# Performance work log

Measured on AMD Instinct MI355X. Metric: run time of the kernel, lower is better.

## Reference

```python
import jax, jax.numpy as jnp
import numpy as np

EPS_BN = 1e-3   # nn.BatchNorm1d(eps=0.001)
LAMDA = 1e-5    # Point_Attentation.lamda


def _bn(x, g, b, m, v):
    # inference-mode BatchNorm1d over last dim
    return (x - m) * (g * jax.lax.rsqrt(v + EPS_BN)) + b


def _forward(features_low, features_high,
             bott_W, bott_b, bott_gamma, bott_beta, bott_mean, bott_var,
             qkv_W, qkv_gamma, qkv_beta, qkv_mean, qkv_var,
             mlp_W, mlp_gamma, mlp_beta, mlp_mean, mlp_var,
             fus_W, fus_b, fus_gamma, fus_beta, fus_mean, fus_var,
             batch_size):
    N, C = features_low.shape
    B = batch_size
    n = N // B  # points per batch segment (equal-length segments)

    # ---- Point_Attentation: per-point channel mean, var over channels / (n-1) ----
    x = features_low
    mean = jnp.mean(x, axis=-1, keepdims=True)
    d = x - mean
    var = jnp.sum(d * d, axis=-1, keepdims=True) / (n - 1)
    e_t = d * d / (4.0 * (var + LAMDA)) + 0.5
    x = x + jax.nn.sigmoid(e_t) * x

    for i in range(3):
        y = jax.nn.relu(_bn(x @ bott_W[2 * i] + bott_b[2 * i],
                            bott_gamma[2 * i], bott_beta[2 * i], bott_mean[2 * i], bott_var[2 * i]))
        y = jax.nn.relu(_bn(y @ bott_W[2 * i + 1] + bott_b[2 * i + 1],
                            bott_gamma[2 * i + 1], bott_beta[2 * i + 1], bott_mean[2 * i + 1], bott_var[2 * i + 1]))
        x = x + y

    # ---- fusion: per-batch QKV attention between low (x) and high features ----
    low = x.reshape(B, n, C)
    high = features_high.reshape(B, n, C)

    q = _bn(jnp.einsum('bnc,cd->bnd', low, qkv_W[0]), qkv_gamma[0], qkv_beta[0], qkv_mean[0], qkv_var[0])
    k = _bn(jnp.einsum('bnc,cd->bnd', high, qkv_W[1]), qkv_gamma[1], qkv_beta[1], qkv_mean[1], qkv_var[1])
    v = _bn(jnp.einsum('bnc,cd->bnd', high, qkv_W[2]), qkv_gamma[2], qkv_beta[2], qkv_mean[2], qkv_var[2])

    scale = 1.0 / jnp.sqrt(jnp.asarray(256.0, dtype=q.dtype))  # normal_dim = 256
    attn = jax.nn.softmax(jnp.einsum('bqc,bkc->bqk', q, k) * scale, axis=-1)
    ao = jnp.einsum('bqk,bkc->bqc', attn, v)

    # mlp: (Linear no-bias -> BN -> Dropout(eval=id) -> ReLU) x2
    h = jax.nn.relu(_bn(jnp.einsum('bnc,cd->bnd', ao, mlp_W[0]), mlp_gamma[0], mlp_beta[0], mlp_mean[0], mlp_var[0]))
    h = jax.nn.relu(_bn(jnp.einsum('bnc,cd->bnd', h, mlp_W[1]), mlp_gamma[1], mlp_beta[1], mlp_mean[1], mlp_var[1]))

    # linear_fusion: Linear(2C->C, bias) -> BN -> ReLU
    cat = jnp.concatenate([low, h], axis=-1)  # [B, n, 2C]
    out = jax.nn.relu(_bn(jnp.einsum('bnc,cd->bnd', cat, fus_W) + fus_b, fus_gamma, fus_beta, fus_mean, fus_var))
    return out.reshape(N, C)


def setup_inputs() -> dict:
    key = jax.random.key(0)
    ks = jax.random.split(key, 16)
    N, C, B = 16384, 256, 4
    s = 0.05
    d = {}
    d['features_low'] = jax.random.normal(ks[0], (N, C), jnp.float32)
    d['features_high'] = jax.random.normal(ks[1], (N, C), jnp.float32)
    d['bott_W'] = jax.random.normal(ks[2], (6, C, C), jnp.float32) * s
    d['bott_b'] = jnp.zeros((6, C), jnp.float32)
    d['bott_gamma'] = jnp.ones((6, C), jnp.float32)
    d['bott_beta'] = jnp.zeros((6, C), jnp.float32)
    d['bott_mean'] = jnp.zeros((6, C), jnp.float32)
    d['bott_var'] = jnp.ones((6, C), jnp.float32)
    d['qkv_W'] = jax.random.normal(ks[3], (3, C, C), jnp.float32) * s
    d['qkv_gamma'] = jnp.ones((3, C), jnp.float32)
    d['qkv_beta'] = jnp.zeros((3, C), jnp.float32)
    d['qkv_mean'] = jnp.zeros((3, C), jnp.float32)
    d['qkv_var'] = jnp.ones((3, C), jnp.float32)
    d['mlp_W'] = jax.random.normal(ks[4], (2, C, C), jnp.float32) * s
    d['mlp_gamma'] = jnp.ones((2, C), jnp.float32)
    d['mlp_beta'] = jnp.zeros((2, C), jnp.float32)
    d['mlp_mean'] = jnp.zeros((2, C), jnp.float32)
    d['mlp_var'] = jnp.ones((2, C), jnp.float32)
    d['fus_W'] = jax.random.normal(ks[5], (2 * C, C), jnp.float32) * s
    d['fus_b'] = jnp.zeros((C,), jnp.float32)
    d['fus_gamma'] = jnp.ones((C,), jnp.float32)
    d['fus_beta'] = jnp.zeros((C,), jnp.float32)
    d['fus_mean'] = jnp.zeros((C,), jnp.float32)
    d['fus_var'] = jnp.ones((C,), jnp.float32)
    d['batch_size'] = B
    return d


def reference(features_low, features_high,
              bott_W, bott_b, bott_gamma, bott_beta, bott_mean, bott_var,
              qkv_W, qkv_gamma, qkv_beta, qkv_mean, qkv_var,
              mlp_W, mlp_gamma, mlp_beta, mlp_mean, mlp_var,
              fus_W, fus_b, fus_gamma, fus_beta, fus_mean, fus_var,
              batch_size):
    return _forward(features_low, features_high,
                    bott_W, bott_b, bott_gamma, bott_beta, bott_mean, bott_var,
                    qkv_W, qkv_gamma, qkv_beta, qkv_mean, qkv_var,
                    mlp_W, mlp_gamma, mlp_beta, mlp_mean, mlp_var,
                    fus_W, fus_b, fus_gamma, fus_beta, fus_mean, fus_var,
                    batch_size)
```

## Files before the change

### kernel.cpp

```cpp
#include <hip/hip_runtime.h>
#include <cstdint>
#include <cstddef>

typedef float v4f __attribute__((ext_vector_type(4)));
typedef float v2f __attribute__((ext_vector_type(2)));
typedef short v8s __attribute__((ext_vector_type(8)));
typedef unsigned short v4u __attribute__((ext_vector_type(4)));

typedef unsigned short ubf;

#define NPTS 16384
#define CD   256
#define NBAT 4
#define NPB  4096

__device__ __forceinline__ float bf2f(ubf u) {
    union { unsigned u; float f; } c; c.u = ((unsigned)u) << 16; return c.f;
}
__device__ __forceinline__ ubf f2bf(float f) {
    union { float f; unsigned u; } c; c.f = f;
    unsigned u = c.u;
    u += 0x7fffu + ((u >> 16) & 1u);
    return (ubf)(u >> 16);
}

__global__ void k_wtrans(const float* __restrict__ bott, const float* __restrict__ qkv,
                         const float* __restrict__ mlp, const float* __restrict__ fus,
                         ubf* __restrict__ wt) {
    const int z = blockIdx.z;
    const float* src; int K; size_t doff;
    if (z < 6)       { src = bott + (size_t)z * 65536;       K = 256; doff = (size_t)z * 65536; }
    else if (z < 9)  { src = qkv  + (size_t)(z - 6) * 65536; K = 256; doff = (size_t)z * 65536; }
    else if (z < 11) { src = mlp  + (size_t)(z - 9) * 65536; K = 256; doff = (size_t)z * 65536; }
    else             { src = fus;                            K = 512; doff = (size_t)11 * 65536; }
    const int kt = blockIdx.y * 32, nt = blockIdx.x * 32;
    if (kt >= K) return;
    __shared__ ubf tile[32][33];
    const int tx = threadIdx.x, ty = threadIdx.y;
#pragma unroll
    for (int i = 0; i < 4; ++i)
        tile[ty * 4 + i][tx] = f2bf(src[(size_t)(kt + ty * 4 + i) * 256 + nt + tx]);
    __syncthreads();
    ubf* dst = wt + doff;
#pragma unroll
    for (int i = 0; i < 4; ++i)
        dst[(size_t)(nt + ty * 4 + i) * K + kt + tx] = tile[tx][ty * 4 + i];
}

__global__ __launch_bounds__(256) void k_point_attn(const float* __restrict__ low,
                                                    float* __restrict__ xout) {
    const int lane = threadIdx.x & 63;
    const int row  = blockIdx.x * 4 + (threadIdx.x >> 6);
    const float* p = low + (size_t)row * CD + lane * 4;
    v4f v = *reinterpret_cast<const v4f*>(p);
    float d[4];
    float s = v[0] + v[1] + v[2] + v[3];
#pragma unroll
    for (int o = 32; o >= 1; o >>= 1) s += __shfl_xor(s, o);
    const float mean = s * (1.0f / 256.0f);
    float ss = 0.f;
#pragma unroll
    for (int i = 0; i < 4; ++i) { d[i] = v[i] - mean; ss += d[i] * d[i]; }
#pragma unroll
    for (int o = 32; o >= 1; o >>= 1) ss += __shfl_xor(ss, o);
    const float var = ss * (1.0f / 4095.0f);
    const float dn  = 1.0f / (4.0f * (var + 1e-5f));
    v4f o;
#pragma unroll
    for (int i = 0; i < 4; ++i) {
        const float e   = d[i] * d[i] * dn + 0.5f;
        const float sig = 1.0f / (1.0f + __expf(-e));
        o[i] = v[i] * (1.0f + sig);
    }
    *reinterpret_cast<v4f*>(xout + (size_t)row * CD + lane * 4) = o;
}

template<int ASRC, bool BIAS, bool RELU, bool RES, int OUT>
__global__ __launch_bounds__(256) void k_gemm(
    const ubf* __restrict__ Abf, const float* __restrict__ Af, const ubf* __restrict__ A2,
    const ubf* __restrict__ WT, const int K,
    const float* __restrict__ bias, const float* __restrict__ gamma, const float* __restrict__ beta,
    const float* __restrict__ bmean, const float* __restrict__ bvar,
    const float* __restrict__ resid, float* __restrict__ outf, ubf* __restrict__ outb) {
    const int lane = threadIdx.x & 63;
    const int w    = threadIdx.x >> 6;
    const int wr = w >> 1, wc = w & 1;
    const int q15 = lane & 15, g = lane >> 4;
    const int bm = blockIdx.x * 128, bn = blockIdx.y * 128;
    const int r0 = bm + wr * 64 + q15;
    const int c0 = bn + wc * 64 + q15;

    v4f acc[4][4];
#pragma unroll
    for (int i = 0; i < 4; ++i)
#pragma unroll
        for (int j = 0; j < 4; ++j)
#pragma unroll
            for (int r = 0; r < 4; ++r) acc[i][j][r] = 0.f;

    const int nk = K >> 5;
    for (int ks = 0; ks < nk; ++ks) {
        const int k0 = ks * 32 + g * 8;
        v8s afr[4], bfr[4];
#pragma unroll
        for (int mi = 0; mi < 4; ++mi) {
            const int row = r0 + mi * 16;
            if constexpr (ASRC == 0) {
                afr[mi] = *reinterpret_cast<const v8s*>(Abf + (size_t)row * K + k0);
            } else if constexpr (ASRC == 1) {
                const float* ap = Af + (size_t)row * CD + k0;
                v4f a = *reinterpret_cast<const v4f*>(ap);
                v4f b = *reinterpret_cast<const v4f*>(ap + 4);
                v8s t;
#pragma unroll
                for (int j = 0; j < 4; ++j) { t[j] = (short)f2bf(a[j]); t[j + 4] = (short)f2bf(b[j]); }
                afr[mi] = t;
            } else {
                if (k0 < 256) {
                    const float* ap = Af + (size_t)row * CD + k0;
                    v4f a = *reinterpret_cast<const v4f*>(ap);
                    v4f b = *reinterpret_cast<const v4f*>(ap + 4);
                    v8s t;
#pragma unroll
                    for (int j = 0; j < 4; ++j) { t[j] = (short)f2bf(a[j]); t[j + 4] = (short)f2bf(b[j]); }
                    afr[mi] = t;
                } else {
                    afr[mi] = *reinterpret_cast<const v8s*>(A2 + (size_t)row * CD + (k0 - 256));
                }
            }
        }
#pragma unroll
        for (int ni = 0; ni < 4; ++ni)
            bfr[ni] = *reinterpret_cast<const v8s*>(WT + (size_t)(c0 + ni * 16) * K + k0);
#pragma unroll
        for (int mi = 0; mi < 4; ++mi)
#pragma unroll
            for (int ni = 0; ni < 4; ++ni)
                acc[mi][ni] = __builtin_amdgcn_mfma_f32_16x16x32_bf16(afr[mi], bfr[ni], acc[mi][ni], 0, 0, 0);
    }

#pragma unroll
    for (int ni = 0; ni < 4; ++ni) {
        const int col = c0 + ni * 16;
        const float sc  = gamma[col] * rsqrtf(bvar[col] + 1e-3f);
        const float tc  = beta[col] - bmean[col] * sc;
        const float bia = BIAS ? bias[col] : 0.f;
#pragma unroll
        for (int mi = 0; mi < 4; ++mi) {
#pragma unroll
            for (int r = 0; r < 4; ++r) {
                const int row = bm + wr * 64 + mi * 16 + g * 4 + r;
                float z = acc[mi][ni][r] + bia;
                z = z * sc + tc;
                if (RELU) z = fmaxf(z, 0.f);
                if (RES)  z += resid[(size_t)row * CD + col];
                if constexpr (OUT == 1) outf[(size_t)row * CD + col] = z;
                else                    outb[(size_t)row * CD + col] = f2bf(z);
            }
        }
    }
}

__global__ __launch_bounds__(256) void k_qkv(
    const float* __restrict__ xA, const float* __restrict__ fh,
    const ubf* __restrict__ wTq,
    const float* __restrict__ qg, const float* __restrict__ qbe,
    const float* __restrict__ qm, const float* __restrict__ qv,
    ubf* __restrict__ qB, ubf* __restrict__ kB, ubf* __restrict__ vT) {
    const int m = blockIdx.y >> 1;
    const float* Af = (m == 0) ? xA : fh;
    const ubf* WT = wTq + m * 65536;
    const float* gamma = qg + m * 256;
    const float* beta  = qbe + m * 256;
    const float* bmean = qm + m * 256;
    const float* bvar  = qv + m * 256;

    const int lane = threadIdx.x & 63;
    const int w    = threadIdx.x >> 6;
    const int wr = w >> 1, wc = w & 1;
    const int q15 = lane & 15, g = lane >> 4;
    const int bm = blockIdx.x * 128, bn = (blockIdx.y & 1) * 128;
    const int r0 = bm + wr * 64 + q15;
    const int c0 = bn + wc * 64 + q15;

    v4f acc[4][4];
#pragma unroll
    for (int i = 0; i < 4; ++i)
#pragma unroll
        for (int j = 0; j < 4; ++j)
#pragma unroll
            for (int r = 0; r < 4; ++r) acc[i][j][r] = 0.f;

    for (int ks = 0; ks < 8; ++ks) {
        const int k0 = ks * 32 + g * 8;
        v8s afr[4], bfr[4];
#pragma unroll
        for (int mi = 0; mi < 4; ++mi) {
            const float* ap = Af + (size_t)(r0 + mi * 16) * CD + k0;
            v4f a = *reinterpret_cast<const v4f*>(ap);
            v4f b = *reinterpret_cast<const v4f*>(ap + 4);
            v8s t;
#pragma unroll
            for (int j = 0; j < 4; ++j) { t[j] = (short)f2bf(a[j]); t[j + 4] = (short)f2bf(b[j]); }
            afr[mi] = t;
        }
#pragma unroll
        for (int ni = 0; ni < 4; ++ni)
            bfr[ni] = *reinterpret_cast<const v8s*>(WT + (size_t)(c0 + ni * 16) * 256 + k0);
#pragma unroll
        for (int mi = 0; mi < 4; ++mi)
#pragma unroll
            for (int ni = 0; ni < 4; ++ni)
                acc[mi][ni] = __builtin_amdgcn_mfma_f32_16x16x32_bf16(afr[mi], bfr[ni], acc[mi][ni], 0, 0, 0);
    }

    ubf* outb = (m == 0) ? qB : kB;
#pragma unroll
    for (int ni = 0; ni < 4; ++ni) {
        const int col = c0 + ni * 16;
        const float sc = gamma[col] * rsqrtf(bvar[col] + 1e-3f);
        const float tc = beta[col] - bmean[col] * sc;
#pragma unroll
        for (int mi = 0; mi < 4; ++mi) {
            if (m == 2) {
                const int row0 = bm + wr * 64 + mi * 16 + g * 4;
                v4u pk;
#pragma unroll
                for (int r = 0; r < 4; ++r) pk[r] = f2bf(acc[mi][ni][r] * sc + tc);
                const int bb = row0 >> 12, key = row0 & 4095;
                *reinterpret_cast<v4u*>(vT + ((size_t)(bb * CD + col)) * NPB + key) = pk;
            } else {
#pragma unroll
                for (int r = 0; r < 4; ++r) {
                    const int row = bm + wr * 64 + mi * 16 + g * 4 + r;
                    outb[(size_t)row * CD + col] = f2bf(acc[mi][ni][r] * sc + tc);
                }
            }
        }
    }
}

__device__ __forceinline__ void stage_kv(const ubf* __restrict__ kg, const ubf* __restrict__ vg,
                                         ubf* kd, ubf* vd, int wave, int lane) {
#pragma unroll
    for (int it = 0; it < 8; ++it) {
        const int Lb = it * 2048 + wave * 512;
        const int L  = Lb + lane * 8;
        {
            const int key = L >> 8, c8 = L & 255;
            const ubf* src = kg + key * CD + (c8 ^ ((key & 7) << 3));
            __builtin_amdgcn_global_load_lds(
                (const __attribute__((address_space(1))) unsigned*)src,
                (__attribute__((address_space(3))) unsigned*)(kd + Lb), 16, 0, 0);
        }
        {
            const int c = L >> 6, k8 = L & 63;
            const ubf* src = vg + (size_t)c * NPB + (k8 ^ ((c & 7) << 3));
            __builtin_amdgcn_global_load_lds(
                (const __attribute__((address_space(1))) unsigned*)src,
                (__attribute__((address_space(3))) unsigned*)(vd + Lb), 16, 0, 0);
        }
    }
}

__global__ __launch_bounds__(256) void k_attn(const ubf* __restrict__ qb, const ubf* __restrict__ kb,
                                              const ubf* __restrict__ vt,
                                              ubf* __restrict__ o0, ubf* __restrict__ o1,
                                              float* __restrict__ ml) {
    __shared__ __attribute__((aligned(16))) ubf kls[64 * 256];
    __shared__ __attribute__((aligned(16))) ubf vls[256 * 64];
    __shared__ __attribute__((aligned(16))) ubf pls[4 * 16 * 64];

    const int raw = blockIdx.x;
    const int xcd = raw & 7, qt = raw >> 3;
    const int b = xcd >> 1, half = xcd & 1;

    const int wave = threadIdx.x >> 6, lane = threadIdx.x & 63;
    const int q15 = lane & 15, g = lane >> 4;

    const ubf* qrow = qb + ((size_t)(b * NPB + qt * 64 + wave * 16 + q15)) * CD + g * 8;
    v8s qf[8];
#pragma unroll
    for (int cs = 0; cs < 8; ++cs) qf[cs] = *reinterpret_cast<const v8s*>(qrow + cs * 32);

    v4f oacc[16];
#pragma unroll
    for (int i = 0; i < 16; ++i)
#pragma unroll
        for (int r = 0; r < 4; ++r) oacc[i][r] = 0.f;
    float m_run = -3.0e38f, l_run = 0.f;

    const ubf* kgb = kb + ((size_t)(b * NPB) + half * 2048) * CD;
    const ubf* vgb = vt + (size_t)b * CD * NPB + half * 2048;
    ubf* pw = pls + wave * 1024;

    for (int kc = 0; kc < 32; ++kc) {
        stage_kv(kgb + (size_t)kc * 64 * CD, vgb + kc * 64, kls, vls, wave, lane);
        __syncthreads();

        v4f sacc[4];
#pragma unroll
        for (int f = 0; f < 4; ++f)
#pragma unroll
            for (int r = 0; r < 4; ++r) sacc[f][r] = 0.f;
#pragma unroll
        for (int cs = 0; cs < 8; ++cs)
#pragma unroll
            for (int f = 0; f < 4; ++f) {
                const int key = 16 * f + q15;
                v8s af = *reinterpret_cast<const v8s*>(&kls[(key * CD + cs * 32 + g * 8) ^ ((key & 7) << 3)]);
                sacc[f] = __builtin_amdgcn_mfma_f32_16x16x32_bf16(af, qf[cs], sacc[f], 0, 0, 0);
            }

        float mloc = -3.0e38f;
#pragma unroll
        for (int f = 0; f < 4; ++f)
#pragma unroll
            for (int r = 0; r < 4; ++r) {
                float x = sacc[f][r] * 0.0625f;
                sacc[f][r] = x;
                mloc = fmaxf(mloc, x);
            }
        mloc = fmaxf(mloc, __shfl_xor(mloc, 16));
        mloc = fmaxf(mloc, __shfl_xor(mloc, 32));
        if (!__all(mloc <= m_run + 8.0f)) {
            const float mnew  = fmaxf(m_run, mloc);
            const float alpha = __expf(m_run - mnew);
            l_run *= alpha;
#pragma unroll
            for (int i = 0; i < 16; ++i)
#pragma unroll
                for (int r = 0; r < 4; ++r) oacc[i][r] *= alpha;
            m_run = mnew;
        }
        float lloc = 0.f;
#pragma unroll
        for (int f = 0; f < 4; ++f)
#pragma unroll
            for (int r = 0; r < 4; ++r) {
                float p = __expf(sacc[f][r] - m_run);
                sacc[f][r] = p;
                lloc += p;
            }
        lloc += __shfl_xor(lloc, 16);
        lloc += __shfl_xor(lloc, 32);
        l_run += lloc;

#pragma unroll
        for (int f = 0; f < 4; ++f) {
            unsigned u0, u1, u2, u3;
            { union { float f; unsigned u; } c; c.f = sacc[f][0]; u0 = c.u; }
            { union { float f; unsigned u; } c; c.f = sacc[f][1]; u1 = c.u; }
            { union { float f; unsigned u; } c; c.f = sacc[f][2]; u2 = c.u; }
            { union { float f; unsigned u; } c; c.f = sacc[f][3]; u3 = c.u; }
            unsigned p01 = (u0 >> 16) | (u1 & 0xFFFF0000u);
            unsigned p23 = (u2 >> 16) | (u3 & 0xFFFF0000u);
            const int e = q15 * 64 + 16 * f + 4 * g;
            *reinterpret_cast<unsigned*>(&pw[(e)     ^ ((q15 & 7) << 3)]) = p01;
            *reinterpret_cast<unsigned*>(&pw[(e + 2) ^ ((q15 & 7) << 3)]) = p23;
        }
        v8s pb0 = *reinterpret_cast<const v8s*>(&pw[(q15 * 64 +  0 + 8 * g) ^ ((q15 & 7) << 3)]);
        v8s pb1 = *reinterpret_cast<const v8s*>(&pw[(q15 * 64 + 32 + 8 * g) ^ ((q15 & 7) << 3)]);
#pragma unroll
        for (int mt = 0; mt < 16; ++mt) {
            const int c = 16 * mt + q15;
            v8s av0 = *reinterpret_cast<const v8s*>(&vls[(c * 64 +  0 + 8 * g) ^ ((c & 7) << 3)]);
            oacc[mt] = __builtin_amdgcn_mfma_f32_16x16x32_bf16(av0, pb0, oacc[mt], 0, 0, 0);
            v8s av1 = *reinterpret_cast<const v8s*>(&vls[(c * 64 + 32 + 8 * g) ^ ((c & 7) << 3)]);
            oacc[mt] = __builtin_amdgcn_mfma_f32_16x16x32_bf16(av1, pb1, oacc[mt], 0, 0, 0);
        }

        __syncthreads();
    }

    const int grow = b * NPB + qt * 64 + wave * 16 + q15;
    ubf* aor = (half ? o1 : o0) + (size_t)grow * CD;
#pragma unroll
    for (int mt = 0; mt < 16; ++mt) {
        v4u pk;
#pragma unroll
        for (int r = 0; r < 4; ++r) pk[r] = f2bf(oacc[mt][r]);
        *reinterpret_cast<v4u*>(aor + 16 * mt + 4 * g) = pk;
    }
    if (g == 0) {
        v2f d; d[0] = m_run; d[1] = l_run;
        *reinterpret_cast<v2f*>(ml + (size_t)(half * NPTS + grow) * 2) = d;
    }
}

__global__ __launch_bounds__(256) void k_merge(ubf* __restrict__ o0, const ubf* __restrict__ o1,
                                               const float* __restrict__ ml) {
    const int row  = blockIdx.x * 4 + (threadIdx.x >> 6);
    const int lane = threadIdx.x & 63;
    v2f a = *reinterpret_cast<const v2f*>(ml + (size_t)row * 2);
    v2f c = *reinterpret_cast<const v2f*>(ml + (size_t)(NPTS + row) * 2);
    const float mx = fmaxf(a[0], c[0]);
    const float w0 = __expf(a[0] - mx), w1 = __expf(c[0] - mx);
    const float inv = 1.0f / (w0 * a[1] + w1 * c[1]);
    ubf* p0 = o0 + (size_t)row * CD + lane * 4;
    const ubf* p1 = o1 + (size_t)row * CD + lane * 4;
    v4u u0 = *reinterpret_cast<const v4u*>(p0);
    v4u u1 = *reinterpret_cast<const v4u*>(p1);
    v4u o;
#pragma unroll
    for (int r = 0; r < 4; ++r)
        o[r] = f2bf((w0 * bf2f(u0[r]) + w1 * bf2f(u1[r])) * inv);
    *reinterpret_cast<v4u*>(p0) = o;
}

extern "C" void kernel_launch(void* const* d_in, const int* in_sizes, int n_in,
                              void* d_out, int out_size, void* d_ws, size_t ws_size,
                              hipStream_t stream) {
    const float* f_low   = (const float*)d_in[0];
    const float* f_high  = (const float*)d_in[1];
    const float* bott_W  = (const float*)d_in[2];
    const float* bott_b  = (const float*)d_in[3];
    const float* bott_g  = (const float*)d_in[4];
    const float* bott_be = (const float*)d_in[5];
    const float* bott_m  = (const float*)d_in[6];
    const float* bott_v  = (const float*)d_in[7];
    const float* qkv_W   = (const float*)d_in[8];
    const float* qkv_g   = (const float*)d_in[9];
    const float* qkv_be  = (const float*)d_in[10];
    const float* qkv_m   = (const float*)d_in[11];
    const float* qkv_v   = (const float*)d_in[12];
    const float* mlp_W   = (const float*)d_in[13];
    const float* mlp_g   = (const float*)d_in[14];
    const float* mlp_be  = (const float*)d_in[15];
    const float* mlp_m   = (const float*)d_in[16];
    const float* mlp_v   = (const float*)d_in[17];
    const float* fus_W   = (const float*)d_in[18];
    const float* fus_b   = (const float*)d_in[19];
    const float* fus_g   = (const float*)d_in[20];
    const float* fus_be  = (const float*)d_in[21];
    const float* fus_m   = (const float*)d_in[22];
    const float* fus_v   = (const float*)d_in[23];
    (void)in_sizes; (void)n_in; (void)out_size; (void)ws_size;

    char* ws = (char*)d_ws;
    const size_t MB = 1024 * 1024;
    float* xA = (float*)(ws);
    ubf*   y  = (ubf*)  (ws + 17 * MB);
    ubf*   qB = (ubf*)  (ws + 26 * MB);
    ubf*   kB = (ubf*)  (ws + 35 * MB);
    ubf*   vT = (ubf*)  (ws + 44 * MB);
    ubf*   wT = (ubf*)  (ws + 53 * MB);
    ubf*   o1 = (ubf*)  (ws + 56 * MB);
    float* ml = (float*)(ws + 65 * MB);

    k_wtrans<<<dim3(8, 16, 12), dim3(32, 8), 0, stream>>>(bott_W, qkv_W, mlp_W, fus_W, wT);
    k_point_attn<<<dim3(4096), dim3(256), 0, stream>>>(f_low, xA);

    const dim3 gg(128, 2), tb(256);
    for (int i = 0; i < 3; ++i) {
        k_gemm<1, true, true, false, 0><<<gg, tb, 0, stream>>>(
            nullptr, xA, nullptr, wT + (size_t)(2 * i) * 65536, 256,
            bott_b + 2 * i * 256, bott_g + 2 * i * 256, bott_be + 2 * i * 256,
            bott_m + 2 * i * 256, bott_v + 2 * i * 256, nullptr, nullptr, y);
        k_gemm<0, true, true, true, 1><<<gg, tb, 0, stream>>>(
            y, nullptr, nullptr, wT + (size_t)(2 * i + 1) * 65536, 256,
            bott_b + (2 * i + 1) * 256, bott_g + (2 * i + 1) * 256, bott_be + (2 * i + 1) * 256,
            bott_m + (2 * i + 1) * 256, bott_v + (2 * i + 1) * 256, xA, xA, nullptr);
    }

    k_qkv<<<dim3(128, 6), tb, 0, stream>>>(xA, f_high, wT + (size_t)6 * 65536,
                                           qkv_g, qkv_be, qkv_m, qkv_v, qB, kB, vT);

    k_attn<<<dim3(512), tb, 0, stream>>>(qB, kB, vT, y, o1, ml);
    k_merge<<<dim3(4096), tb, 0, stream>>>(y, o1, ml);

    k_gemm<0, false, true, false, 0><<<gg, tb, 0, stream>>>(
        y, nullptr, nullptr, wT + (size_t)9 * 65536, 256,
        nullptr, mlp_g + 0, mlp_be + 0, mlp_m + 0, mlp_v + 0, nullptr, nullptr, qB);
    k_gemm<0, false, true, false, 0><<<gg, tb, 0, stream>>>(
        qB, nullptr, nullptr, wT + (size_t)10 * 65536, 256,
        nullptr, mlp_g + 256, mlp_be + 256, mlp_m + 256, mlp_v + 256, nullptr, nullptr, kB);

    k_gemm<2, true, true, false, 1><<<gg, tb, 0, stream>>>(
        nullptr, xA, kB, wT + (size_t)11 * 65536, 512,
        fus_b, fus_g, fus_be, fus_m, fus_v, nullptr, (float*)d_out, nullptr);
}
```

Measured before the change: 348.7 us.

## Fuse preprocessing kernels, fold split-KV merge into MLP GEMM, read V directly

Merges the weight-transpose and point-attention kernels into one launch, and folds the split-KV softmax merge into the A-operand load of the first MLP GEMM. This removes a launch and a full read-modify-write pass over the attention output. The attention kernel now stages only K in shared memory, loading V fragments straight from global memory. K staging for the next chunk is issued after the score MFMAs, so the loads can overlap the softmax work. The merge math is redone per column tile (twice), and uncached global V reads may raise latency in the PV loop.

```diff
diff --git a/kernel.cpp b/kernel.cpp
--- a/kernel.cpp
+++ b/kernel.cpp
@@ -24,19 +24,50 @@
     return (ubf)(u >> 16);
 }
 
-__global__ void k_wtrans(const float* __restrict__ bott, const float* __restrict__ qkv,
-                         const float* __restrict__ mlp, const float* __restrict__ fus,
-                         ubf* __restrict__ wt) {
-    const int z = blockIdx.z;
+__global__ __launch_bounds__(256) void k_pre(
+    const float* __restrict__ low, float* __restrict__ xout,
+    const float* __restrict__ bott, const float* __restrict__ qkv,
+    const float* __restrict__ mlp, const float* __restrict__ fus,
+    ubf* __restrict__ wt) {
+    const int bid = blockIdx.x;
+    if (bid < 4096) {
+        const int lane = threadIdx.x & 63;
+        const int row  = bid * 4 + (threadIdx.x >> 6);
+        const float* p = low + (size_t)row * CD + lane * 4;
+        v4f v = *reinterpret_cast<const v4f*>(p);
+        float d[4];
+        float s = v[0] + v[1] + v[2] + v[3];
+#pragma unroll
+        for (int o = 32; o >= 1; o >>= 1) s += __shfl_xor(s, o);
+        const float mean = s * (1.0f / 256.0f);
+        float ss = 0.f;
+#pragma unroll
+        for (int i = 0; i < 4; ++i) { d[i] = v[i] - mean; ss += d[i] * d[i]; }
+#pragma unroll
+        for (int o = 32; o >= 1; o >>= 1) ss += __shfl_xor(ss, o);
+        const float var = ss * (1.0f / 4095.0f);
+        const float dn  = 1.0f / (4.0f * (var + 1e-5f));
+        v4f o;
+#pragma unroll
+        for (int i = 0; i < 4; ++i) {
+            const float e   = d[i] * d[i] * dn + 0.5f;
+            const float sig = 1.0f / (1.0f + __expf(-e));
+            o[i] = v[i] * (1.0f + sig);
+        }
+        *reinterpret_cast<v4f*>(xout + (size_t)row * CD + lane * 4) = o;
+        return;
+    }
+    const int bid2 = bid - 4096;
+    const int z = bid2 >> 7, r = bid2 & 127;
     const float* src; int K; size_t doff;
     if (z < 6)       { src = bott + (size_t)z * 65536;       K = 256; doff = (size_t)z * 65536; }
     else if (z < 9)  { src = qkv  + (size_t)(z - 6) * 65536; K = 256; doff = (size_t)z * 65536; }
     else if (z < 11) { src = mlp  + (size_t)(z - 9) * 65536; K = 256; doff = (size_t)z * 65536; }
     else             { src = fus;                            K = 512; doff = (size_t)11 * 65536; }
-    const int kt = blockIdx.y * 32, nt = blockIdx.x * 32;
+    const int kt = (r >> 3) * 32, nt = (r & 7) * 32;
     if (kt >= K) return;
     __shared__ ubf tile[32][33];
-    const int tx = threadIdx.x, ty = threadIdx.y;
+    const int tx = threadIdx.x & 31, ty = threadIdx.x >> 5;
 #pragma unroll
     for (int i = 0; i < 4; ++i)
         tile[ty * 4 + i][tx] = f2bf(src[(size_t)(kt + ty * 4 + i) * 256 + nt + tx]);
@@ -45,34 +76,6 @@
 #pragma unroll
     for (int i = 0; i < 4; ++i)
         dst[(size_t)(nt + ty * 4 + i) * K + kt + tx] = tile[tx][ty * 4 + i];
-}
-
-__global__ __launch_bounds__(256) void k_point_attn(const float* __restrict__ low,
-                                                    float* __restrict__ xout) {
-    const int lane = threadIdx.x & 63;
-    const int row  = blockIdx.x * 4 + (threadIdx.x >> 6);
-    const float* p = low + (size_t)row * CD + lane * 4;
-    v4f v = *reinterpret_cast<const v4f*>(p);
-    float d[4];
-    float s = v[0] + v[1] + v[2] + v[3];
-#pragma unroll
-    for (int o = 32; o >= 1; o >>= 1) s += __shfl_xor(s, o);
-    const float mean = s * (1.0f / 256.0f);
-    float ss = 0.f;
-#pragma unroll
-    for (int i = 0; i < 4; ++i) { d[i] = v[i] - mean; ss += d[i] * d[i]; }
-#pragma unroll
-    for (int o = 32; o >= 1; o >>= 1) ss += __shfl_xor(ss, o);
-    const float var = ss * (1.0f / 4095.0f);
-    const float dn  = 1.0f / (4.0f * (var + 1e-5f));
-    v4f o;
-#pragma unroll
-    for (int i = 0; i < 4; ++i) {
-        const float e   = d[i] * d[i] * dn + 0.5f;
-        const float sig = 1.0f / (1.0f + __expf(-e));
-        o[i] = v[i] * (1.0f + sig);
-    }
-    *reinterpret_cast<v4f*>(xout + (size_t)row * CD + lane * 4) = o;
 }
 
 template<int ASRC, bool BIAS, bool RELU, bool RES, int OUT>
@@ -98,6 +101,20 @@
 #pragma unroll
             for (int r = 0; r < 4; ++r) acc[i][j][r] = 0.f;
 
+    float a0[4], a1[4];
+    if constexpr (ASRC == 3) {
+#pragma unroll
+        for (int mi = 0; mi < 4; ++mi) {
+            const int row = r0 + mi * 16;
+            const float m0 = resid[2 * row],          l0 = resid[2 * row + 1];
+            const float m1 = resid[2 * (NPTS + row)], l1 = resid[2 * (NPTS + row) + 1];
+            const float mx = fmaxf(m0, m1);
+            const float w0 = __expf(m0 - mx), w1 = __expf(m1 - mx);
+            const float inv = 1.0f / (w0 * l0 + w1 * l1);
+            a0[mi] = w0 * inv; a1[mi] = w1 * inv;
+        }
+    }
+
     const int nk = K >> 5;
     for (int ks = 0; ks < nk; ++ks) {
         const int k0 = ks * 32 + g * 8;
@@ -114,6 +131,14 @@
                 v8s t;
 #pragma unroll
                 for (int j = 0; j < 4; ++j) { t[j] = (short)f2bf(a[j]); t[j + 4] = (short)f2bf(b[j]); }
+                afr[mi] = t;
+            } else if constexpr (ASRC == 3) {
+                v8s u0 = *reinterpret_cast<const v8s*>(Abf + (size_t)row * CD + k0);
+                v8s u1 = *reinterpret_cast<const v8s*>(A2 + (size_t)row * CD + k0);
+                v8s t;
+#pragma unroll
+                for (int j = 0; j < 8; ++j)
+                    t[j] = (short)f2bf(a0[mi] * bf2f((ubf)u0[j]) + a1[mi] * bf2f((ubf)u1[j]));
                 afr[mi] = t;
             } else {
                 if (k0 < 256) {
@@ -240,26 +265,17 @@
     }
 }
 
-__device__ __forceinline__ void stage_kv(const ubf* __restrict__ kg, const ubf* __restrict__ vg,
-                                         ubf* kd, ubf* vd, int wave, int lane) {
+__device__ __forceinline__ void stage_k(const ubf* __restrict__ kg,
+                                        ubf* kd, int wave, int lane) {
 #pragma unroll
     for (int it = 0; it < 8; ++it) {
         const int Lb = it * 2048 + wave * 512;
         const int L  = Lb + lane * 8;
-        {
-            const int key = L >> 8, c8 = L & 255;
-            const ubf* src = kg + key * CD + (c8 ^ ((key & 7) << 3));
-            __builtin_amdgcn_global_load_lds(
-                (const __attribute__((address_space(1))) unsigned*)src,
-                (__attribute__((address_space(3))) unsigned*)(kd + Lb), 16, 0, 0);
-        }
-        {
-            const int c = L >> 6, k8 = L & 63;
-            const ubf* src = vg + (size_t)c * NPB + (k8 ^ ((c & 7) << 3));
-            __builtin_amdgcn_global_load_lds(
-                (const __attribute__((address_space(1))) unsigned*)src,
-                (__attribute__((address_space(3))) unsigned*)(vd + Lb), 16, 0, 0);
-        }
+        const int key = L >> 8, c8 = L & 255;
+        const ubf* src = kg + key * CD + (c8 ^ ((key & 7) << 3));
+        __builtin_amdgcn_global_load_lds(
+            (const __attribute__((address_space(1))) unsigned*)src,
+            (__attribute__((address_space(3))) unsigned*)(kd + Lb), 16, 0, 0);
     }
 }
 
@@ -268,7 +284,6 @@
                                               ubf* __restrict__ o0, ubf* __restrict__ o1,
                                               float* __restrict__ ml) {
     __shared__ __attribute__((aligned(16))) ubf kls[64 * 256];
-    __shared__ __attribute__((aligned(16))) ubf vls[256 * 64];
     __shared__ __attribute__((aligned(16))) ubf pls[4 * 16 * 64];
 
     const int raw = blockIdx.x;
@@ -294,10 +309,10 @@
     const ubf* vgb = vt + (size_t)b * CD * NPB + half * 2048;
     ubf* pw = pls + wave * 1024;
 
+    stage_k(kgb, kls, wave, lane);
+    __syncthreads();
+
     for (int kc = 0; kc < 32; ++kc) {
-        stage_kv(kgb + (size_t)kc * 64 * CD, vgb + kc * 64, kls, vls, wave, lane);
-        __syncthreads();
-
         v4f sacc[4];
 #pragma unroll
         for (int f = 0; f < 4; ++f)
@@ -311,6 +326,10 @@
                 v8s af = *reinterpret_cast<const v8s*>(&kls[(key * CD + cs * 32 + g * 8) ^ ((key & 7) << 3)]);
                 sacc[f] = __builtin_amdgcn_mfma_f32_16x16x32_bf16(af, qf[cs], sacc[f], 0, 0, 0);
             }
+
+        __syncthreads();
+        if (kc + 1 < 32)
+            stage_k(kgb + (size_t)(kc + 1) * 64 * CD, kls, wave, lane);
 
         float mloc = -3.0e38f;
 #pragma unroll
@@ -363,10 +382,10 @@
         v8s pb1 = *reinterpret_cast<const v8s*>(&pw[(q15 * 64 + 32 + 8 * g) ^ ((q15 & 7) << 3)]);
 #pragma unroll
         for (int mt = 0; mt < 16; ++mt) {
-            const int c = 16 * mt + q15;
-            v8s av0 = *reinterpret_cast<const v8s*>(&vls[(c * 64 +  0 + 8 * g) ^ ((c & 7) << 3)]);
+            const ubf* vrow = vgb + (size_t)(16 * mt + q15) * NPB + kc * 64;
+            v8s av0 = *reinterpret_cast<const v8s*>(vrow + 8 * g);
             oacc[mt] = __builtin_amdgcn_mfma_f32_16x16x32_bf16(av0, pb0, oacc[mt], 0, 0, 0);
-            v8s av1 = *reinterpret_cast<const v8s*>(&vls[(c * 64 + 32 + 8 * g) ^ ((c & 7) << 3)]);
+            v8s av1 = *reinterpret_cast<const v8s*>(vrow + 32 + 8 * g);
             oacc[mt] = __builtin_amdgcn_mfma_f32_16x16x32_bf16(av1, pb1, oacc[mt], 0, 0, 0);
         }
 
@@ -386,26 +405,6 @@
         v2f d; d[0] = m_run; d[1] = l_run;
         *reinterpret_cast<v2f*>(ml + (size_t)(half * NPTS + grow) * 2) = d;
     }
-}
-
-__global__ __launch_bounds__(256) void k_merge(ubf* __restrict__ o0, const ubf* __restrict__ o1,
-                                               const float* __restrict__ ml) {
-    const int row  = blockIdx.x * 4 + (threadIdx.x >> 6);
-    const int lane = threadIdx.x & 63;
-    v2f a = *reinterpret_cast<const v2f*>(ml + (size_t)row * 2);
-    v2f c = *reinterpret_cast<const v2f*>(ml + (size_t)(NPTS + row) * 2);
-    const float mx = fmaxf(a[0], c[0]);
-    const float w0 = __expf(a[0] - mx), w1 = __expf(c[0] - mx);
-    const float inv = 1.0f / (w0 * a[1] + w1 * c[1]);
-    ubf* p0 = o0 + (size_t)row * CD + lane * 4;
-    const ubf* p1 = o1 + (size_t)row * CD + lane * 4;
-    v4u u0 = *reinterpret_cast<const v4u*>(p0);
-    v4u u1 = *reinterpret_cast<const v4u*>(p1);
-    v4u o;
-#pragma unroll
-    for (int r = 0; r < 4; ++r)
-        o[r] = f2bf((w0 * bf2f(u0[r]) + w1 * bf2f(u1[r])) * inv);
-    *reinterpret_cast<v4u*>(p0) = o;
 }
 
 extern "C" void kernel_launch(void* const* d_in, const int* in_sizes, int n_in,
@@ -448,8 +447,8 @@
     ubf*   o1 = (ubf*)  (ws + 56 * MB);
     float* ml = (float*)(ws + 65 * MB);
 
-    k_wtrans<<<dim3(8, 16, 12), dim3(32, 8), 0, stream>>>(bott_W, qkv_W, mlp_W, fus_W, wT);
-    k_point_attn<<<dim3(4096), dim3(256), 0, stream>>>(f_low, xA);
+    k_pre<<<dim3(4096 + 1536), dim3(256), 0, stream>>>(f_low, xA,
+                                                       bott_W, qkv_W, mlp_W, fus_W, wT);
 
     const dim3 gg(128, 2), tb(256);
     for (int i = 0; i < 3; ++i) {
@@ -467,11 +466,10 @@
                                            qkv_g, qkv_be, qkv_m, qkv_v, qB, kB, vT);
 
     k_attn<<<dim3(512), tb, 0, stream>>>(qB, kB, vT, y, o1, ml);
-    k_merge<<<dim3(4096), tb, 0, stream>>>(y, o1, ml);
-
-    k_gemm<0, false, true, false, 0><<<gg, tb, 0, stream>>>(
-        y, nullptr, nullptr, wT + (size_t)9 * 65536, 256,
-        nullptr, mlp_g + 0, mlp_be + 0, mlp_m + 0, mlp_v + 0, nullptr, nullptr, qB);
+
+    k_gemm<3, false, true, false, 0><<<gg, tb, 0, stream>>>(
+        y, nullptr, o1, wT + (size_t)9 * 65536, 256,
+        nullptr, mlp_g + 0, mlp_be + 0, mlp_m + 0, mlp_v + 0, ml, nullptr, qB);
     k_gemm<0, false, true, false, 0><<<gg, tb, 0, stream>>>(
         qB, nullptr, nullptr, wT + (size_t)10 * 65536, 256,
         nullptr, mlp_g + 256, mlp_be + 256, mlp_m + 256, mlp_v + 256, nullptr, nullptr, kB);
```

New measurement: 502.0 us. 1.44x slower.
